# Kernel tuning notes

Measured on AMD Instinct MI355X. Metric: run time of the kernel, lower is better.

## Reference

```python
import jax, jax.numpy as jnp
import numpy as np

N, F_IN, H, O = 4096, 512, 4, 256
ALPHA = 0.2  # leaky-relu negative slope
NEG = -9e15  # mask value for non-edges (matches DAEGC)


def setup_inputs() -> dict:
    key = jax.random.key(0)
    ks = jax.random.split(key, 9)
    x = jax.random.normal(ks[0], (N, F_IN), jnp.float32)
    adj = (jax.random.uniform(ks[1], (N, N)) < 0.01).astype(jnp.float32)
    adj = jnp.maximum(adj, jnp.eye(N, dtype=jnp.float32))
    M = jax.random.uniform(ks[2], (N, N), dtype=jnp.float32)  # proximity matrix
    s0 = 1.0 / np.sqrt(F_IN)
    s1 = 1.0 / np.sqrt(H * O)
    W0 = jax.random.normal(ks[3], (H, F_IN, O), jnp.float32) * s0
    a_self0 = jax.random.normal(ks[4], (H, O), jnp.float32) * 0.1
    a_neigh0 = jax.random.normal(ks[5], (H, O), jnp.float32) * 0.1
    W1 = jax.random.normal(ks[6], (H, H * O, O), jnp.float32) * s1
    a_self1 = jax.random.normal(ks[7], (H, O), jnp.float32) * 0.1
    a_neigh1 = jax.random.normal(ks[8], (H, O), jnp.float32) * 0.1
    return dict(x=x, adj=adj, M=M, W0=W0, a_self0=a_self0, a_neigh0=a_neigh0,
                W1=W1, a_self1=a_self1, a_neigh1=a_neigh1)


def gat_layer(x, adj, M, W, a_s, a_n, concat):
    # x: [N, F_in], W: [H, F_in, O]
    h = jnp.einsum('nf,hfo->hno', x, W)                      # [H, N, O]
    e = (jnp.einsum('hno,ho->hn', h, a_s)[:, :, None]
         + jnp.einsum('hno,ho->hn', h, a_n)[:, None, :])     # [H, N, N]
    e = jax.nn.leaky_relu(e * M[None], ALPHA)
    e = jnp.where(adj[None] > 0, e, NEG)
    attn = jax.nn.softmax(e, axis=-1)                        # masked neighbor softmax
    out = jnp.einsum('hnm,hmo->hno', attn, h)                # [H, N, O]
    if concat:
        return jax.nn.elu(out.transpose(1, 0, 2).reshape(x.shape[0], -1))  # [N, H*O]
    return out.mean(axis=0)                                  # [N, O]


def reference(x, adj, M, W0, a_self0, a_neigh0, W1, a_self1, a_neigh1):
    h = gat_layer(x, adj, M, W0, a_self0, a_neigh0, True)
    h = gat_layer(h, adj, M, W1, a_self1, a_neigh1, False)
    # F.normalize(h, p=2, dim=1) with eps=1e-12
    z = h / jnp.maximum(jnp.linalg.norm(h, axis=1, keepdims=True), 1e-12)
    A_pred = jax.nn.sigmoid(z @ z.T)                          # dot-product decode [N, N]
    return (A_pred, z)
```

## Files before the change

kernel.cpp:

```cpp
#include <hip/hip_runtime.h>
#include <hip/hip_bf16.h>
#include <math.h>

#define N_NODES 4096
#define F_IN0   512
#define HEADS   4
#define O_DIM   256
#define HO      1024
#define LRELU_A 0.2f
#define MAXE    192
#define LOG2E   1.44269504088896f

typedef __bf16 bf16_t;
typedef bf16_t bf16x8 __attribute__((ext_vector_type(8)));
typedef float f32x4 __attribute__((ext_vector_type(4)));
typedef unsigned short u16x8 __attribute__((ext_vector_type(8)));

__device__ __forceinline__ unsigned short f2b(float f) {
    __hip_bfloat16 t = __float2bfloat16(f);
    return __builtin_bit_cast(unsigned short, t);
}
__device__ __forceinline__ float b2f(unsigned short u) {
    unsigned int v = ((unsigned int)u) << 16;
    return __builtin_bit_cast(float, v);
}
__device__ __forceinline__ float fexp(float x) {
    return __builtin_amdgcn_exp2f(x * LOG2E);
}
__device__ __forceinline__ float fsigmoid(float x) {
    return __builtin_amdgcn_rcpf(1.f + __builtin_amdgcn_exp2f(-x * LOG2E));
}

#define GLOAD_LDS(g, l) \
    __builtin_amdgcn_global_load_lds((const __attribute__((address_space(1))) unsigned int*)(g), \
                                     (__attribute__((address_space(3))) unsigned int*)(l), 16, 0, 0)

__device__ __forceinline__ void transpose_tile(const float* __restrict__ W,
                                               unsigned short* __restrict__ Wt,
                                               int K, int O, int kt, int ot, int h,
                                               float (*t)[33], int tid) {
    const float* Wh = W + (size_t)h * K * O;
    unsigned short* Wth = Wt + (size_t)h * K * O;
    const int k0 = kt * 32, o0 = ot * 32;
    const int tx = tid & 31, ty = tid >> 5;
    for (int r = ty; r < 32; r += 8) t[r][tx] = Wh[(size_t)(k0 + r) * O + o0 + tx];
    __syncthreads();
    for (int r = ty; r < 32; r += 8)
        Wth[(size_t)(o0 + r) * K + k0 + tx] = f2b(t[tx][r]);
}

__global__ __launch_bounds__(256) void prep_k(const float* __restrict__ x,
                                              const float* __restrict__ W0,
                                              const float* __restrict__ W1,
                                              const float* __restrict__ adj,
                                              const float* __restrict__ Mm,
                                              unsigned short* __restrict__ xb,
                                              unsigned short* __restrict__ wt0,
                                              unsigned short* __restrict__ wt1,
                                              int* __restrict__ ecnt,
                                              int* __restrict__ eidx,
                                              float* __restrict__ eMv) {
    __shared__ float t[32][33];
    __shared__ int cnt;
    const int b = blockIdx.x;
    const int tid = threadIdx.x;
    if (b < 2048) {
        int i = b * 256 + tid;
        float4 v = ((const float4*)x)[i];
        ushort4 o;
        o.x = f2b(v.x); o.y = f2b(v.y); o.z = f2b(v.z); o.w = f2b(v.w);
        ((ushort4*)xb)[i] = o;
    } else if (b < 2560) {
        int b2 = b - 2048;
        transpose_tile(W0, wt0, F_IN0, O_DIM, (b2 & 15), ((b2 >> 4) & 7), b2 >> 7, t, tid);
    } else if (b < 3584) {
        int b2 = b - 2560;
        transpose_tile(W1, wt1, HO, O_DIM, (b2 & 31), ((b2 >> 5) & 7), b2 >> 8, t, tid);
    } else {
        const int n = b - 3584;
        if (tid == 0) cnt = 0;
        __syncthreads();
        const float* adjr = adj + (size_t)n * N_NODES;
        const float* Mr   = Mm  + (size_t)n * N_NODES;
        for (int m0 = tid * 4; m0 < N_NODES; m0 += 1024) {
            const float4 a4 = *(const float4*)&adjr[m0];
            const float av[4] = {a4.x, a4.y, a4.z, a4.w};
#pragma unroll
            for (int q = 0; q < 4; ++q) {
                if (av[q] > 0.f) {
                    int m = m0 + q;
                    int k = atomicAdd(&cnt, 1);
                    eidx[(size_t)n * MAXE + k] = m;
                    eMv[(size_t)n * MAXE + k]  = Mr[m];
                }
            }
        }
        __syncthreads();
        if (tid == 0) ecnt[n] = cnt;
    }
}

__global__ __launch_bounds__(256) void mfma_nt(const bf16_t* __restrict__ A,
                                               const bf16_t* __restrict__ B,
                                               unsigned short* __restrict__ Cv,
                                               int K, int ldc,
                                               unsigned long long bStride,
                                               unsigned long long cStride) {
    B += blockIdx.z * bStride;
    const size_t zoff = (size_t)blockIdx.z * cStride;
    __shared__ bf16_t sA[128 * 32];
    __shared__ bf16_t sB[128 * 32];
    const int tid  = threadIdx.x;
    const int lane = tid & 63;
    const int wave = tid >> 6;
    const int wr = (wave >> 1) * 64;
    const int wc = (wave & 1) * 64;
    const int rowBase = blockIdx.x * 128;
    const int colBase = blockIdx.y * 128;
    const int l15  = lane & 15;
    const int quad = lane >> 4;

    const int sm = tid & 127;
    const int sc = tid >> 7;
    const bf16_t* aRow = A + (size_t)(rowBase + sm) * K + sc * 8;
    const bf16_t* bRow = B + (size_t)(colBase + sm) * K + sc * 8;
    bf16_t* sA0 = &sA[(tid & ~63) * 8];
    bf16_t* sA1 = &sA[(256 + (tid & ~63)) * 8];
    bf16_t* sB0 = &sB[(tid & ~63) * 8];
    bf16_t* sB1 = &sB[(256 + (tid & ~63)) * 8];

    f32x4 acc[4][4] = {};

    for (int k0 = 0; k0 < K; k0 += 32) {
        GLOAD_LDS(aRow + k0,      sA0);
        GLOAD_LDS(aRow + k0 + 16, sA1);
        GLOAD_LDS(bRow + k0,      sB0);
        GLOAD_LDS(bRow + k0 + 16, sB1);
        __syncthreads();
        bf16x8 af[4], bfr[4];
#pragma unroll
        for (int i = 0; i < 4; ++i) {
            af[i]  = *(bf16x8*)&sA[(quad * 128 + wr + i * 16 + l15) * 8];
            bfr[i] = *(bf16x8*)&sB[(quad * 128 + wc + i * 16 + l15) * 8];
        }
#pragma unroll
        for (int i = 0; i < 4; ++i)
#pragma unroll
            for (int j = 0; j < 4; ++j)
                acc[i][j] = __builtin_amdgcn_mfma_f32_16x16x32_bf16(af[i], bfr[j], acc[i][j], 0, 0, 0);
        __syncthreads();
    }

    const int orow = rowBase + wr + quad * 4;
    const int ocol = colBase + wc + l15;
#pragma unroll
    for (int i = 0; i < 4; ++i)
#pragma unroll
        for (int j = 0; j < 4; ++j)
#pragma unroll
            for (int r = 0; r < 4; ++r)
                Cv[zoff + (size_t)(orow + i * 16 + r) * ldc + ocol + j * 16] = f2b(acc[i][j][r]);
}

__global__ __launch_bounds__(256) void decode_k(const bf16_t* __restrict__ Z,
                                                float* __restrict__ out) {
    const int tid  = threadIdx.x;
    const int lane = tid & 63;
    const int wave = tid >> 6;
    const int rowBase = blockIdx.x * 128 + (wave >> 1) * 64;
    const int colBase = blockIdx.y * 128 + (wave & 1) * 64;
    const int l15  = lane & 15;
    const int quad = lane >> 4;
    const bf16_t* aBase = Z + (size_t)(rowBase + l15) * O_DIM + quad * 8;
    const bf16_t* bBase = Z + (size_t)(colBase + l15) * O_DIM + quad * 8;

    f32x4 acc[4][4] = {};
#pragma unroll
    for (int kc = 0; kc < 8; ++kc) {
        bf16x8 a[4], b[4];
#pragma unroll
        for (int i = 0; i < 4; ++i) {
            a[i] = *(const bf16x8*)(aBase + (size_t)i * 16 * O_DIM + kc * 32);
            b[i] = *(const bf16x8*)(bBase + (size_t)i * 16 * O_DIM + kc * 32);
        }
#pragma unroll
        for (int i = 0; i < 4; ++i)
#pragma unroll
            for (int j = 0; j < 4; ++j)
                acc[i][j] = __builtin_amdgcn_mfma_f32_16x16x32_bf16(a[i], b[j], acc[i][j], 0, 0, 0);
    }

    const int orow = rowBase + quad * 4;
    const int ocol = colBase + l15;
#pragma unroll
    for (int i = 0; i < 4; ++i)
#pragma unroll
        for (int j = 0; j < 4; ++j)
#pragma unroll
            for (int r = 0; r < 4; ++r)
                out[(size_t)(orow + i * 16 + r) * N_NODES + ocol + j * 16] =
                    fsigmoid(acc[i][j][r]);
}

__global__ __launch_bounds__(256) void scores_k(const unsigned short* __restrict__ hb,
                                                const float* __restrict__ a_s,
                                                const float* __restrict__ a_n,
                                                float* __restrict__ s_self4,
                                                float* __restrict__ s_neigh4) {
    const int n = blockIdx.x;
    const int head = threadIdx.x >> 6;
    const int lane = threadIdx.x & 63;
    const ushort4 hv = *(const ushort4*)&hb[(size_t)n * HO + head * O_DIM + lane * 4];
    const float4 av = *(const float4*)&a_s[head * O_DIM + lane * 4];
    const float4 nv = *(const float4*)&a_n[head * O_DIM + lane * 4];
    float h0 = b2f(hv.x), h1 = b2f(hv.y), h2 = b2f(hv.z), h3 = b2f(hv.w);
    float ps = h0 * av.x + h1 * av.y + h2 * av.z + h3 * av.w;
    float pn = h0 * nv.x + h1 * nv.y + h2 * nv.z + h3 * nv.w;
    for (int off = 32; off; off >>= 1) {
        ps += __shfl_down(ps, off, 64);
        pn += __shfl_down(pn, off, 64);
    }
    if (lane == 0) {
        s_self4[n * HEADS + head]  = ps;
        s_neigh4[n * HEADS + head] = pn;
    }
}

__global__ __launch_bounds__(256) void attn_k(const unsigned short* __restrict__ hb,
                                              const int* __restrict__ ecnt,
                                              const int* __restrict__ eidx,
                                              const float* __restrict__ eMv,
                                              const float* __restrict__ s_self4,
                                              const float* __restrict__ s_neigh4,
                                              unsigned short* __restrict__ out0,
                                              float* __restrict__ out1, int layer) {
    const int n = blockIdx.x;
    const int tid = threadIdx.x;
    __shared__ int midx[MAXE];
    __shared__ float ev[MAXE][HEADS];
    __shared__ float red2[2][HO];
    const int c = ecnt[n];

    if (tid < c) {
        const int m = eidx[(size_t)n * MAXE + tid];
        const float Mv = eMv[(size_t)n * MAXE + tid];
        midx[tid] = m;
        const float4 ss = *(const float4*)&s_self4[n * HEADS];
        const float4 sn = *(const float4*)&s_neigh4[m * HEADS];
        float e0 = (ss.x + sn.x) * Mv, e1 = (ss.y + sn.y) * Mv;
        float e2 = (ss.z + sn.z) * Mv, e3 = (ss.w + sn.w) * Mv;
        ev[tid][0] = e0 > 0.f ? e0 : LRELU_A * e0;
        ev[tid][1] = e1 > 0.f ? e1 : LRELU_A * e1;
        ev[tid][2] = e2 > 0.f ? e2 : LRELU_A * e2;
        ev[tid][3] = e3 > 0.f ? e3 : LRELU_A * e3;
    }
    __syncthreads();

    {
        const int w = tid >> 6, lane = tid & 63;
        float mx = -1e30f;
        for (int k = lane; k < c; k += 64) mx = fmaxf(mx, ev[k][w]);
        for (int off = 32; off; off >>= 1) mx = fmaxf(mx, __shfl_xor(mx, off, 64));
        float s = 0.f;
        for (int k = lane; k < c; k += 64) {
            float p = fexp(ev[k][w] - mx);
            ev[k][w] = p;
            s += p;
        }
        for (int off = 32; off; off >>= 1) s += __shfl_xor(s, off, 64);
        float inv = __builtin_amdgcn_rcpf(s);
        for (int k = lane; k < c; k += 64) ev[k][w] *= inv;
    }
    __syncthreads();

    const int half = tid >> 7;
    const int t    = tid & 127;
    const int hh   = t >> 5;
    float acc[8] = {};
#pragma unroll 2
    for (int k = half; k < c; k += 2) {
        const int m = midx[k];
        const float w = ev[k][hh];
        const u16x8 hv = *(const u16x8*)&hb[(size_t)m * HO + t * 8];
#pragma unroll
        for (int j = 0; j < 8; ++j) acc[j] += w * b2f(hv[j]);
    }
#pragma unroll
    for (int j = 0; j < 8; ++j) red2[half][t * 8 + j] = acc[j];
    __syncthreads();

    if (layer == 0) {
        const int o = tid * 4;
        ushort4 ov;
        float v0 = red2[0][o + 0] + red2[1][o + 0];
        float v1 = red2[0][o + 1] + red2[1][o + 1];
        float v2 = red2[0][o + 2] + red2[1][o + 2];
        float v3 = red2[0][o + 3] + red2[1][o + 3];
        ov.x = f2b(v0 > 0.f ? v0 : fexp(v0) - 1.f);
        ov.y = f2b(v1 > 0.f ? v1 : fexp(v1) - 1.f);
        ov.z = f2b(v2 > 0.f ? v2 : fexp(v2) - 1.f);
        ov.w = f2b(v3 > 0.f ? v3 : fexp(v3) - 1.f);
        *(ushort4*)&out0[(size_t)n * HO + o] = ov;
    } else {
        const int o = tid;
        float v = 0.f;
#pragma unroll
        for (int h = 0; h < HEADS; ++h)
            v += red2[0][h * O_DIM + o] + red2[1][h * O_DIM + o];
        out1[(size_t)n * O_DIM + o] = 0.25f * v;
    }
}

__global__ __launch_bounds__(256) void norm_k(float* __restrict__ z,
                                              unsigned short* __restrict__ zb) {
    const int n = blockIdx.x;
    const int tid = threadIdx.x;
    float v = z[(size_t)n * O_DIM + tid];
    float p = v * v;
    for (int off = 32; off; off >>= 1) p += __shfl_down(p, off, 64);
    __shared__ float wsum[4];
    if ((tid & 63) == 0) wsum[tid >> 6] = p;
    __syncthreads();
    float ssq = wsum[0] + wsum[1] + wsum[2] + wsum[3];
    float denom = fmaxf(sqrtf(ssq), 1e-12f);
    float zn = v / denom;
    z[(size_t)n * O_DIM + tid] = zn;
    zb[(size_t)n * O_DIM + tid] = f2b(zn);
}

extern "C" void kernel_launch(void* const* d_in, const int* in_sizes, int n_in,
                              void* d_out, int out_size, void* d_ws, size_t ws_size,
                              hipStream_t stream) {
    const float* x   = (const float*)d_in[0];
    const float* adj = (const float*)d_in[1];
    const float* Mm  = (const float*)d_in[2];
    const float* W0  = (const float*)d_in[3];
    const float* as0 = (const float*)d_in[4];
    const float* an0 = (const float*)d_in[5];
    const float* W1  = (const float*)d_in[6];
    const float* as1 = (const float*)d_in[7];
    const float* an1 = (const float*)d_in[8];
    float* out = (float*)d_out;

    unsigned short* hb    = (unsigned short*)d_ws;
    unsigned short* hin1b = hb + (size_t)N_NODES * HO;
    unsigned short* xb    = hin1b + (size_t)N_NODES * HO;
    unsigned short* wt0   = xb + (size_t)N_NODES * F_IN0;
    unsigned short* wt1   = wt0 + HEADS * O_DIM * F_IN0;
    unsigned short* zb    = wt1 + HEADS * O_DIM * HO;
    float* s_self4  = (float*)(zb + (size_t)N_NODES * O_DIM);
    float* s_neigh4 = s_self4 + N_NODES * HEADS;
    int*   eidx = (int*)(s_neigh4 + N_NODES * HEADS);
    float* eMv  = (float*)(eidx + (size_t)N_NODES * MAXE);
    int*   ecnt = (int*)(eMv + (size_t)N_NODES * MAXE);
    float* zbuf = out + (size_t)N_NODES * N_NODES;

    prep_k<<<7680, 256, 0, stream>>>(x, W0, W1, adj, Mm, xb, wt0, wt1, ecnt, eidx, eMv);

    mfma_nt<<<dim3(32, 2, 4), 256, 0, stream>>>((const bf16_t*)xb, (const bf16_t*)wt0, hb,
                                                F_IN0, HO,
                                                (unsigned long long)O_DIM * F_IN0,
                                                (unsigned long long)O_DIM);
    scores_k<<<N_NODES, 256, 0, stream>>>(hb, as0, an0, s_self4, s_neigh4);
    attn_k<<<N_NODES, 256, 0, stream>>>(hb, ecnt, eidx, eMv, s_self4, s_neigh4, hin1b, nullptr, 0);

    mfma_nt<<<dim3(32, 2, 4), 256, 0, stream>>>((const bf16_t*)hin1b, (const bf16_t*)wt1, hb,
                                                HO, HO,
                                                (unsigned long long)O_DIM * HO,
                                                (unsigned long long)O_DIM);
    scores_k<<<N_NODES, 256, 0, stream>>>(hb, as1, an1, s_self4, s_neigh4);
    attn_k<<<N_NODES, 256, 0, stream>>>(hb, ecnt, eidx, eMv, s_self4, s_neigh4, nullptr, zbuf, 1);

    norm_k<<<N_NODES, 256, 0, stream>>>(zbuf, zb);
    decode_k<<<dim3(32, 32), 256, 0, stream>>>((const bf16_t*)zb, out);
}
```

Baseline: 336.4 us.

## Stage decode operands in LDS and coalesce sigmoid output via shared-memory epilogue

The dot-product decode kernel now loads Z tiles into LDS with direct global-to-LDS loads instead of each wave reading its fragments straight from global memory. The epilogue writes accumulators to a padded LDS buffer and then stores 16-byte vectorized rows of sigmoid outputs. This is meant to fix the scattered 4-byte stores to the large 4096x4096 fp32 output, which dominate this kernel's memory traffic. In exchange it adds several block-wide barriers and LDS round trips, and the LDS buffer is reused across operand staging and the epilogue.

```diff
diff --git a/kernel.cpp b/kernel.cpp
--- a/kernel.cpp
+++ b/kernel.cpp
@@ -162,44 +162,77 @@
                 Cv[zoff + (size_t)(orow + i * 16 + r) * ldc + ocol + j * 16] = f2b(acc[i][j][r]);
 }
 
+#define EP_STRIDE 132
 __global__ __launch_bounds__(256) void decode_k(const bf16_t* __restrict__ Z,
                                                 float* __restrict__ out) {
+    __shared__ float smem_f[32 * EP_STRIDE];
+    bf16_t* sA = (bf16_t*)smem_f;
+    bf16_t* sB = (bf16_t*)(smem_f + 2048);
+    float*  sE = smem_f;
+
     const int tid  = threadIdx.x;
     const int lane = tid & 63;
     const int wave = tid >> 6;
-    const int rowBase = blockIdx.x * 128 + (wave >> 1) * 64;
-    const int colBase = blockIdx.y * 128 + (wave & 1) * 64;
+    const int wr = (wave >> 1) * 64;
+    const int wc = (wave & 1) * 64;
+    const int rowBase = blockIdx.x * 128;
+    const int colBase = blockIdx.y * 128;
     const int l15  = lane & 15;
     const int quad = lane >> 4;
-    const bf16_t* aBase = Z + (size_t)(rowBase + l15) * O_DIM + quad * 8;
-    const bf16_t* bBase = Z + (size_t)(colBase + l15) * O_DIM + quad * 8;
+
+    const int sm = tid & 127;
+    const int sc = tid >> 7;
+    const bf16_t* aRow = Z + (size_t)(rowBase + sm) * O_DIM + sc * 8;
+    const bf16_t* bRow = Z + (size_t)(colBase + sm) * O_DIM + sc * 8;
+    bf16_t* sA0 = &sA[(tid & ~63) * 8];
+    bf16_t* sA1 = &sA[(256 + (tid & ~63)) * 8];
+    bf16_t* sB0 = &sB[(tid & ~63) * 8];
+    bf16_t* sB1 = &sB[(256 + (tid & ~63)) * 8];
 
     f32x4 acc[4][4] = {};
-#pragma unroll
-    for (int kc = 0; kc < 8; ++kc) {
-        bf16x8 a[4], b[4];
+
+    for (int k0 = 0; k0 < O_DIM; k0 += 32) {
+        GLOAD_LDS(aRow + k0,      sA0);
+        GLOAD_LDS(aRow + k0 + 16, sA1);
+        GLOAD_LDS(bRow + k0,      sB0);
+        GLOAD_LDS(bRow + k0 + 16, sB1);
+        __syncthreads();
+        bf16x8 af[4], bfr[4];
 #pragma unroll
         for (int i = 0; i < 4; ++i) {
-            a[i] = *(const bf16x8*)(aBase + (size_t)i * 16 * O_DIM + kc * 32);
-            b[i] = *(const bf16x8*)(bBase + (size_t)i * 16 * O_DIM + kc * 32);
+            af[i]  = *(bf16x8*)&sA[(quad * 128 + wr + i * 16 + l15) * 8];
+            bfr[i] = *(bf16x8*)&sB[(quad * 128 + wc + i * 16 + l15) * 8];
         }
 #pragma unroll
         for (int i = 0; i < 4; ++i)
 #pragma unroll
             for (int j = 0; j < 4; ++j)
-                acc[i][j] = __builtin_amdgcn_mfma_f32_16x16x32_bf16(a[i], b[j], acc[i][j], 0, 0, 0);
-    }
-
-    const int orow = rowBase + quad * 4;
-    const int ocol = colBase + l15;
-#pragma unroll
-    for (int i = 0; i < 4; ++i)
+                acc[i][j] = __builtin_amdgcn_mfma_f32_16x16x32_bf16(af[i], bfr[j], acc[i][j], 0, 0, 0);
+        __syncthreads();
+    }
+
+    const int lrBase = (wave >> 1) * 16;
+    for (int i = 0; i < 4; ++i) {
 #pragma unroll
         for (int j = 0; j < 4; ++j)
 #pragma unroll
             for (int r = 0; r < 4; ++r)
-                out[(size_t)(orow + i * 16 + r) * N_NODES + ocol + j * 16] =
-                    fsigmoid(acc[i][j][r]);
+                sE[(lrBase + quad * 4 + r) * EP_STRIDE + wc + j * 16 + l15] = acc[i][j][r];
+        __syncthreads();
+#pragma unroll
+        for (int p = 0; p < 4; ++p) {
+            const int idx4 = p * 256 + tid;
+            const int lr = idx4 >> 5;
+            const int c4 = idx4 & 31;
+            f32x4 v = *(f32x4*)&sE[lr * EP_STRIDE + c4 * 4];
+            f32x4 o;
+            o[0] = fsigmoid(v[0]); o[1] = fsigmoid(v[1]);
+            o[2] = fsigmoid(v[2]); o[3] = fsigmoid(v[3]);
+            const int grow = rowBase + (lr >> 4) * 64 + i * 16 + (lr & 15);
+            *(f32x4*)&out[(size_t)grow * N_NODES + colBase + c4 * 4] = o;
+        }
+        __syncthreads();
+    }
 }
 
 __global__ __launch_bounds__(256) void scores_k(const unsigned short* __restrict__ hb,
```

Result: faster. 324.0 us (-3.7%).
